# Performance work log

Hardware: AMD Instinct MI355X
Metric: run time of the kernel (lower is better)

The kernel has to match this reference:

```python
import jax, jax.numpy as jnp
import numpy as np

B, N, DIM = 4, 1024, 512
H, DH = 8, 64
INNER = H * DH
MLP = 2048
EPS = 1e-5


def layernorm(x, g, b):
    m = x.mean(-1, keepdims=True)
    v = ((x - m) ** 2).mean(-1, keepdims=True)
    return (x - m) / jnp.sqrt(v + EPS) * g + b


def setup_inputs() -> dict:
    key = jax.random.key(0)
    ks = jax.random.split(key, 12)
    s = 0.02
    return {
        "q": jax.random.normal(ks[0], (B, N, DIM), jnp.float32),
        "k": jax.random.normal(ks[1], (B, N, DIM), jnp.float32),
        "v": jax.random.normal(ks[2], (B, N, DIM), jnp.float32),
        "Win": jax.random.normal(ks[3], (INNER, DIM), jnp.float32) * s,
        "Wout": jax.random.normal(ks[4], (DIM, INNER), jnp.float32) * s,
        "bout": jnp.zeros((DIM,), jnp.float32),
        "g1": jnp.ones((DIM,), jnp.float32),
        "b1n": jnp.zeros((DIM,), jnp.float32),
        "g2": jnp.ones((DIM,), jnp.float32),
        "b2n": jnp.zeros((DIM,), jnp.float32),
        "Wup": jax.random.normal(ks[5], (MLP, DIM), jnp.float32) * s,
        "bup": jnp.zeros((MLP,), jnp.float32),
        "Wdn": jax.random.normal(ks[6], (DIM, MLP), jnp.float32) * s,
        "bdn": jnp.zeros((DIM,), jnp.float32),
        "wp_W1": jax.random.normal(ks[7], (DH, 2 * DH), jnp.float32) * s,
        "wp_b1": jnp.zeros((DH,), jnp.float32),
        "wp_g": jnp.ones((DH,), jnp.float32),
        "wp_b": jnp.zeros((DH,), jnp.float32),
        "wp_W2": jax.random.normal(ks[8], (3, DH), jnp.float32) * s,
        "wp_b2": jnp.zeros((3,), jnp.float32),
        "num_heads": H,
        "dim_head": DH,
        "mlp_dim": MLP,
    }


def reference(q, k, v, Win, Wout, bout, g1, b1n, g2, b2n, Wup, bup, Wdn, bdn,
              wp_W1, wp_b1, wp_g, wp_b, wp_W2, wp_b2, num_heads, dim_head, mlp_dim):
    b, n, _ = q.shape

    def split_heads(x):  # [b,n,dim] -> [h,b,n,d]
        f = x @ Win.T
        return f.reshape(b, n, num_heads, dim_head).transpose(2, 0, 1, 3)

    fq = split_heads(layernorm(q, g1, b1n))
    fk = split_heads(layernorm(k, g1, b1n))
    fv = split_heads(layernorm(v, g1, b1n))

    # cosine similarity component
    dots = jnp.einsum('hbnd,hbmd->hbnm', fq, fk)
    nq = jnp.linalg.norm(fq, axis=-1)  # [h,b,n]
    nk = jnp.linalg.norm(fk, axis=-1)  # [h,b,m]
    cosine_sim = dots / (nq[..., :, None] * nk[..., None, :])

    # mean-centered covariance component
    qc = fq - fq.mean(-1, keepdims=True)
    kc = fk - fk.mean(-1, keepdims=True)
    cov_component = jnp.einsum('hbnd,hbmd->hbnm', qc, kc) / dim_head

    # variance outer-product component (torch.var -> unbiased, ddof=1)
    qv = jnp.var(fq, axis=-1, ddof=1)  # [h,b,n]
    kv = jnp.var(fk, axis=-1, ddof=1)  # [h,b,m]
    var_component = qv[..., :, None] * kv[..., None, :] / dim_head

    # dynamic per-head mixing weights
    qg = fq.mean(axis=(1, 2))  # [h,d]
    kg = fk.mean(axis=(1, 2))
    feats = jnp.concatenate([qg, kg], axis=-1)  # [h,2d]
    h1 = jax.nn.relu(layernorm(feats @ wp_W1.T + wp_b1, wp_g, wp_b))
    w = jax.nn.softmax(h1 @ wp_W2.T + wp_b2, axis=-1)  # [h,3]
    cw = w[:, 0][:, None, None, None]
    covw = w[:, 1][:, None, None, None]
    vw = w[:, 2][:, None, None, None]

    scores = cw * cosine_sim + covw * cov_component + vw * var_component
    out = jnp.einsum('hbnm,hbmd->hbnd', scores, fv)
    out = out.transpose(1, 2, 0, 3).reshape(b, n, num_heads * dim_head)
    attn = out @ Wout.T + bout

    q2 = q + attn
    x = layernorm(q2, g2, b2n)
    y = jax.nn.gelu(x @ Wup.T + bup, approximate=False) @ Wdn.T + bdn
    return q2 + y
```

## Files before the change

kernel.cpp:

```cpp
#include <hip/hip_runtime.h>
#include <math.h>

#define EPS 1e-5f
#define ROWS 4096

typedef __attribute__((ext_vector_type(8))) short short8;
typedef __attribute__((ext_vector_type(4))) float floatx4;

__device__ inline short f2bf(float f) {
    unsigned u = __builtin_bit_cast(unsigned, f);
    unsigned r = (u + 0x7fffu + ((u >> 16) & 1u)) >> 16;
    return (short)r;
}

__global__ __launch_bounds__(256) void lnconv(
    const float* __restrict__ x0, const float* __restrict__ x1,
    const float* __restrict__ x2, const float* __restrict__ g,
    const float* __restrict__ bb, short* __restrict__ out) {
    int tensor = blockIdx.y;
    const float* x = tensor == 0 ? x0 : (tensor == 1 ? x1 : x2);
    int t = threadIdx.x;
    int row = blockIdx.x * 4 + (t >> 6);
    int col = (t & 63) * 8;
    const float* xr = x + (size_t)row * 512 + col;
    float4 v0 = *(const float4*)xr;
    float4 v1 = *(const float4*)(xr + 4);
    float s = v0.x + v0.y + v0.z + v0.w + v1.x + v1.y + v1.z + v1.w;
    float sq = v0.x * v0.x + v0.y * v0.y + v0.z * v0.z + v0.w * v0.w +
               v1.x * v1.x + v1.y * v1.y + v1.z * v1.z + v1.w * v1.w;
#pragma unroll
    for (int off = 32; off; off >>= 1) {
        s += __shfl_xor(s, off);
        sq += __shfl_xor(sq, off);
    }
    float m = s * (1.f / 512.f);
    float rstd = rsqrtf(sq * (1.f / 512.f) - m * m + EPS);
    float4 g0 = *(const float4*)(g + col);
    float4 g1 = *(const float4*)(g + col + 4);
    float4 b0 = *(const float4*)(bb + col);
    float4 b1 = *(const float4*)(bb + col + 4);
    short8 o;
    o[0] = f2bf((v0.x - m) * rstd * g0.x + b0.x);
    o[1] = f2bf((v0.y - m) * rstd * g0.y + b0.y);
    o[2] = f2bf((v0.z - m) * rstd * g0.z + b0.z);
    o[3] = f2bf((v0.w - m) * rstd * g0.w + b0.w);
    o[4] = f2bf((v1.x - m) * rstd * g1.x + b1.x);
    o[5] = f2bf((v1.y - m) * rstd * g1.y + b1.y);
    o[6] = f2bf((v1.z - m) * rstd * g1.z + b1.z);
    o[7] = f2bf((v1.w - m) * rstd * g1.w + b1.w);
    *(short8*)(out + (size_t)(tensor * 4096 + row) * 512 + col) = o;
}

__global__ void wconv(const float* __restrict__ w0, const float* __restrict__ w1,
                      const float* __restrict__ w2, const float* __restrict__ w3,
                      short* __restrict__ o0, short* __restrict__ o1,
                      short* __restrict__ o2, short* __restrict__ o3) {
    int y = blockIdx.y;
    const float* src = y == 0 ? w0 : (y == 1 ? w1 : (y == 2 ? w2 : w3));
    short* dst = y == 0 ? o0 : (y == 1 ? o1 : (y == 2 ? o2 : o3));
    int n = (y < 2) ? 262144 : 1048576;
    int idx = (blockIdx.x * 256 + threadIdx.x) * 8;
    if (idx < n) {
        float4 v0 = *(const float4*)(src + idx);
        float4 v1 = *(const float4*)(src + idx + 4);
        short8 o;
        o[0] = f2bf(v0.x); o[1] = f2bf(v0.y); o[2] = f2bf(v0.z); o[3] = f2bf(v0.w);
        o[4] = f2bf(v1.x); o[5] = f2bf(v1.y); o[6] = f2bf(v1.z); o[7] = f2bf(v1.w);
        *(short8*)(dst + idx) = o;
    }
}

template <int TM, int TN, int EPI, bool OUT_BF16>
__global__ __launch_bounds__(256) void mfma_gemm_nt(
    const short* __restrict__ A, const short* __restrict__ B,
    void* __restrict__ C, int M, int N, int K,
    const float* __restrict__ bias, const float* __restrict__ resid) {
    constexpr int FI = TM / 32;
    constexpr int FJ = TN / 32;
    __shared__ short As[TM * 32];
    __shared__ short Bs[TN * 32];
    int t = threadIdx.x;
    int m0 = blockIdx.y * TM, n0 = blockIdx.x * TN;
    int w = t >> 6, lane = t & 63;
    int wm = (w & 1) * (TM / 2), wn = (w >> 1) * (TN / 2);
    floatx4 acc[FI][FJ];
#pragma unroll
    for (int i = 0; i < FI; ++i)
#pragma unroll
        for (int j = 0; j < FJ; ++j) acc[i][j] = (floatx4){0.f, 0.f, 0.f, 0.f};

    int arow = t >> 2, acol = (t & 3) * 8;
    const short* Ag = A + (size_t)(m0 + arow) * K + acol;
    const short* Bg = B + (size_t)(n0 + arow) * K + acol;
    int ldsbase = w * 1024;

    for (int k0 = 0; k0 < K; k0 += 32) {
        __syncthreads();
#pragma unroll
        for (int u = 0; u < TM / 64; ++u)
            __builtin_amdgcn_global_load_lds(
                (const __attribute__((address_space(1))) void*)(Ag + (size_t)u * 64 * K + k0),
                (__attribute__((address_space(3))) void*)((char*)As + u * 4096 + ldsbase),
                16, 0, 0);
#pragma unroll
        for (int u = 0; u < TN / 64; ++u)
            __builtin_amdgcn_global_load_lds(
                (const __attribute__((address_space(1))) void*)(Bg + (size_t)u * 64 * K + k0),
                (__attribute__((address_space(3))) void*)((char*)Bs + u * 4096 + ldsbase),
                16, 0, 0);
        __syncthreads();
        int krow = (lane >> 4) * 8;
        short8 af[FI], bf[FJ];
#pragma unroll
        for (int i = 0; i < FI; ++i)
            af[i] = *(const short8*)&As[(wm + i * 16 + (lane & 15)) * 32 + krow];
#pragma unroll
        for (int j = 0; j < FJ; ++j)
            bf[j] = *(const short8*)&Bs[(wn + j * 16 + (lane & 15)) * 32 + krow];
#pragma unroll
        for (int i = 0; i < FI; ++i)
#pragma unroll
            for (int j = 0; j < FJ; ++j)
                acc[i][j] = __builtin_amdgcn_mfma_f32_16x16x32_bf16(
                    af[i], bf[j], acc[i][j], 0, 0, 0);
    }

    int col = lane & 15, rbase = (lane >> 4) * 4;
#pragma unroll
    for (int i = 0; i < FI; ++i) {
#pragma unroll
        for (int j = 0; j < FJ; ++j) {
            int gcol = n0 + wn + j * 16 + col;
#pragma unroll
            for (int r = 0; r < 4; ++r) {
                int grow = m0 + wm + i * 16 + rbase + r;
                float v = acc[i][j][r];
                if (EPI == 2) v += bias[gcol] + resid[(size_t)grow * N + gcol];
                if (EPI == 3) {
                    v += bias[gcol];
                    v = 0.5f * v * (1.f + erff(v * 0.70710678118654752f));
                }
                if (OUT_BF16)
                    ((short*)C)[(size_t)grow * N + gcol] = f2bf(v);
                else
                    ((float*)C)[(size_t)grow * N + gcol] = v;
            }
        }
    }
}

__global__ void head_stats2(const float* __restrict__ fq, const float* __restrict__ fk,
                            float* __restrict__ S) {
    int row = blockIdx.x;
    int y = blockIdx.y;
    const float* f = y ? fk : fq;
    float* base = S + (size_t)y * 98304;
    int t = threadIdx.x;
    int h = t >> 6, lane = t & 63;
    float v = f[(size_t)row * 512 + t];
    float s = v, sq = v * v;
#pragma unroll
    for (int off = 32; off; off >>= 1) {
        s += __shfl_xor(s, off);
        sq += __shfl_xor(sq, off);
    }
    if (lane == 0) {
        float m = s * (1.f / 64.f);
        int idx = h * ROWS + row;
        base[idx] = m;
        base[32768 + idx] = rsqrtf(sq);
        base[65536 + idx] = (sq - 64.f * m * m) * (1.f / 63.f);
    }
}

__global__ void zero_k(float* __restrict__ p, int n) {
    int i = blockIdx.x * blockDim.x + threadIdx.x;
    if (i < n) p[i] = 0.f;
}

__global__ void colmean(const float* __restrict__ fq, const float* __restrict__ fk,
                        float* __restrict__ qg, float* __restrict__ kg) {
    int tensor = blockIdx.y;
    const float* f = tensor ? fk : fq;
    float* o = tensor ? kg : qg;
    int col = threadIdx.x;
    int r0 = blockIdx.x * 32;
    float s = 0.f;
    for (int r = 0; r < 32; ++r) s += f[(size_t)(r0 + r) * 512 + col];
    atomicAdd(&o[col], s * (1.f / 4096.f));
}

__global__ void policy_mlp(const float* __restrict__ qg, const float* __restrict__ kg,
                           const float* __restrict__ W1, const float* __restrict__ b1,
                           const float* __restrict__ g, const float* __restrict__ bb,
                           const float* __restrict__ W2, const float* __restrict__ b2,
                           float* __restrict__ wmix) {
    int h = blockIdx.x, j = threadIdx.x;
    float acc = 0.f;
    const float* w1r = W1 + j * 128;
    for (int i = 0; i < 64; ++i) acc += qg[h * 64 + i] * w1r[i];
    for (int i = 0; i < 64; ++i) acc += kg[h * 64 + i] * w1r[64 + i];
    acc += b1[j];
    float s = acc, sq = acc * acc;
#pragma unroll
    for (int off = 32; off; off >>= 1) {
        s += __shfl_xor(s, off);
        sq += __shfl_xor(sq, off);
    }
    float m = s * (1.f / 64.f);
    float var = sq * (1.f / 64.f) - m * m;
    float xh = (acc - m) * rsqrtf(var + EPS) * g[j] + bb[j];
    float r = fmaxf(xh, 0.f);
    float l[3];
#pragma unroll
    for (int c = 0; c < 3; ++c) {
        float p = r * W2[c * 64 + j];
#pragma unroll
        for (int off = 32; off; off >>= 1) p += __shfl_xor(p, off);
        l[c] = p + b2[c];
    }
    if (j == 0) {
        float mx = fmaxf(l[0], fmaxf(l[1], l[2]));
        float e0 = expf(l[0] - mx), e1 = expf(l[1] - mx), e2 = expf(l[2] - mx);
        float inv = 1.f / (e0 + e1 + e2);
        wmix[h * 3 + 0] = e0 * inv;
        wmix[h * 3 + 1] = e1 * inv;
        wmix[h * 3 + 2] = e2 * inv;
    }
}

__global__ __launch_bounds__(256) void ksideP(
    const float* __restrict__ fk, const float* __restrict__ fv,
    const float* __restrict__ rnk, const float* __restrict__ kvv,
    const float* __restrict__ mk, float* __restrict__ Mpart) {
    int hb = blockIdx.x;
    int chunk = blockIdx.y;
    int h = hb >> 2, b = hb & 3;
    __shared__ float fkt[2048], fvt[2048];
    __shared__ float rs[32], kvs[32], mks[32];
    int t = threadIdx.x;
    int td = t >> 4, te = t & 15;
    float m1[4][4] = {}, m2[4][4] = {};
    float skv = 0.f, smk = 0.f;
    int mstart = chunk * 128;
    for (int m0 = mstart; m0 < mstart + 128; m0 += 32) {
        __syncthreads();
#pragma unroll
        for (int u = 0; u < 2; ++u) {
            int idx = u * 1024 + t * 4;
            int mm = idx >> 6, d = idx & 63;
            size_t grow = (size_t)(b * 1024 + m0 + mm) * 512 + h * 64 + d;
            *(float4*)&fkt[idx] = *(const float4*)&fk[grow];
            *(float4*)&fvt[idx] = *(const float4*)&fv[grow];
        }
        if (t < 32) {
            int sidx = h * ROWS + b * 1024 + m0 + t;
            rs[t] = rnk[sidx];
            kvs[t] = kvv[sidx];
            mks[t] = mk[sidx];
        }
        __syncthreads();
        for (int mi = 0; mi < 32; ++mi) {
            float r = rs[mi];
            float4 kq = *(const float4*)&fkt[mi * 64 + td * 4];
            float4 vq = *(const float4*)&fvt[mi * 64 + te * 4];
            float kr[4] = {kq.x, kq.y, kq.z, kq.w};
            float vr[4] = {vq.x, vq.y, vq.z, vq.w};
#pragma unroll
            for (int i = 0; i < 4; ++i) {
                float kv_ = kr[i], krr = kv_ * r;
#pragma unroll
                for (int j = 0; j < 4; ++j) {
                    m2[i][j] += kv_ * vr[j];
                    m1[i][j] += krr * vr[j];
                }
            }
            if (t < 64) {
                skv += kvs[mi] * fvt[mi * 64 + t];
                smk += mks[mi] * fvt[mi * 64 + t];
            }
        }
    }
    float* base = Mpart + (size_t)(chunk * 32 + hb) * 8320;
#pragma unroll
    for (int i = 0; i < 4; ++i)
#pragma unroll
        for (int j = 0; j < 4; ++j) {
            base[(td * 4 + i) * 64 + te * 4 + j] = m1[i][j];
            base[4096 + (td * 4 + i) * 64 + te * 4 + j] = m2[i][j];
        }
    if (t < 64) {
        base[8192 + t] = skv;
        base[8256 + t] = smk;
    }
}

__global__ void reduceM(const float* __restrict__ Mpart, float* __restrict__ Mbuf) {
    int i = blockIdx.x * 256 + threadIdx.x;
    if (i < 32 * 8320) {
        float s = 0.f;
#pragma unroll
        for (int c = 0; c < 8; ++c) s += Mpart[(size_t)c * 266240 + i];
        Mbuf[i] = s;
    }
}

__global__ __launch_bounds__(256) void qside(
    const float* __restrict__ fq, const float* __restrict__ Mbuf,
    const float* __restrict__ rnq, const float* __restrict__ mq,
    const float* __restrict__ qv, const float* __restrict__ wmix,
    short* __restrict__ attn_out) {
    int ntile = blockIdx.x, hb = blockIdx.y;
    int h = hb >> 2, b = hb & 3;
    __shared__ float M1s[4096], M2s[4096], fqt[4096];
    __shared__ float Skvs[64], Smks[64], rnqs[64], mqs[64], qvs[64];
    int t = threadIdx.x;
    const float* base = Mbuf + (size_t)hb * 8320;
#pragma unroll
    for (int u = 0; u < 4; ++u) {
        int idx = t * 4 + u * 1024;
        *(float4*)&M1s[idx] = *(const float4*)&base[idx];
        *(float4*)&M2s[idx] = *(const float4*)&base[4096 + idx];
    }
    int n0 = ntile * 64;
#pragma unroll
    for (int u = 0; u < 4; ++u) {
        int idx = t * 4 + u * 1024;
        int r = idx >> 6, d = idx & 63;
        *(float4*)&fqt[idx] = *(const float4*)&fq[(size_t)(b * 1024 + n0 + r) * 512 + h * 64 + d];
    }
    if (t < 64) {
        Skvs[t] = base[8192 + t];
        Smks[t] = base[8256 + t];
        int sidx = h * ROWS + b * 1024 + n0 + t;
        rnqs[t] = rnq[sidx];
        mqs[t] = mq[sidx];
        qvs[t] = qv[sidx];
    }
    __syncthreads();
    float cw = wmix[h * 3 + 0], covw = wmix[h * 3 + 1], vw = wmix[h * 3 + 2];
    int e = t & 63, rq = t >> 6;
    float a1[16] = {}, a2[16] = {};
    for (int d4 = 0; d4 < 64; d4 += 4) {
        float md1[4], md2[4];
#pragma unroll
        for (int dd = 0; dd < 4; ++dd) {
            md1[dd] = M1s[(d4 + dd) * 64 + e];
            md2[dd] = M2s[(d4 + dd) * 64 + e];
        }
#pragma unroll
        for (int i = 0; i < 16; ++i) {
            float4 f = *(const float4*)&fqt[(rq * 16 + i) * 64 + d4];
            a1[i] += f.x * md1[0] + f.y * md1[1] + f.z * md1[2] + f.w * md1[3];
            a2[i] += f.x * md2[0] + f.y * md2[1] + f.z * md2[2] + f.w * md2[3];
        }
    }
    float c2 = covw * (1.f / 64.f), c3 = vw * (1.f / 64.f);
#pragma unroll
    for (int i = 0; i < 16; ++i) {
        int rr = rq * 16 + i;
        float v = cw * rnqs[rr] * a1[i] + c2 * a2[i] + c3 * qvs[rr] * Skvs[e] -
                  covw * mqs[rr] * Smks[e];
        attn_out[(size_t)(b * 1024 + n0 + rr) * 512 + h * 64 + e] = f2bf(v);
    }
}

extern "C" void kernel_launch(void* const* d_in, const int* in_sizes, int n_in,
                              void* d_out, int out_size, void* d_ws, size_t ws_size,
                              hipStream_t stream) {
    const float* q = (const float*)d_in[0];
    const float* k = (const float*)d_in[1];
    const float* v = (const float*)d_in[2];
    const float* Win = (const float*)d_in[3];
    const float* Wout = (const float*)d_in[4];
    const float* bout = (const float*)d_in[5];
    const float* g1 = (const float*)d_in[6];
    const float* b1n = (const float*)d_in[7];
    const float* g2 = (const float*)d_in[8];
    const float* b2n = (const float*)d_in[9];
    const float* Wup = (const float*)d_in[10];
    const float* bup = (const float*)d_in[11];
    const float* Wdn = (const float*)d_in[12];
    const float* bdn = (const float*)d_in[13];
    const float* wpW1 = (const float*)d_in[14];
    const float* wpb1 = (const float*)d_in[15];
    const float* wpg = (const float*)d_in[16];
    const float* wpb = (const float*)d_in[17];
    const float* wpW2 = (const float*)d_in[18];
    const float* wpb2 = (const float*)d_in[19];
    float* out = (float*)d_out;

    float* wsf = (float*)d_ws;
    float* fq = wsf;
    float* fk = wsf + 2097152;
    float* fv = wsf + 2 * 2097152;
    short* hmid = (short*)wsf;
    short* qkvln = (short*)(wsf + 6291456);
    float* Mpart = wsf + 6291456;
    short* attnbf = (short*)(wsf + 6291456);
    short* x2bf = (short*)(wsf + 6291456 + 1048576);
    short* Winbf = (short*)(wsf + 9437184);
    short* Woutbf = (short*)(wsf + 9437184 + 131072);
    short* Wupbf = (short*)(wsf + 9437184 + 262144);
    short* Wdnbf = (short*)(wsf + 9437184 + 262144 + 524288);
    float* S = wsf + 10747904;
    float* qg = S + 196608;
    float* kg = qg + 512;
    float* Mbuf = kg + 512;
    float* wmix = Mbuf + 266240;
    float* mqS = S, *rnqS = S + 32768, *qvS = S + 65536;
    float* mkS = S + 98304, *rnkS = S + 131072, *kvS = S + 163840;

    wconv<<<dim3(512, 4), 256, 0, stream>>>(Win, Wout, Wup, Wdn,
                                            Winbf, Woutbf, Wupbf, Wdnbf);
    lnconv<<<dim3(1024, 3), 256, 0, stream>>>(q, k, v, g1, b1n, qkvln);
    zero_k<<<4, 256, 0, stream>>>(qg, 1024);

    mfma_gemm_nt<64, 128, 0, false><<<dim3(4, 192), 256, 0, stream>>>(
        qkvln, Winbf, fq, 12288, 512, 512, nullptr, nullptr);

    head_stats2<<<dim3(4096, 2), 512, 0, stream>>>(fq, fk, S);
    colmean<<<dim3(128, 2), 512, 0, stream>>>(fq, fk, qg, kg);
    policy_mlp<<<8, 64, 0, stream>>>(qg, kg, wpW1, wpb1, wpg, wpb, wpW2, wpb2, wmix);

    ksideP<<<dim3(32, 8), 256, 0, stream>>>(fk, fv, rnkS, kvS, mkS, Mpart);
    reduceM<<<1040, 256, 0, stream>>>(Mpart, Mbuf);
    qside<<<dim3(16, 32), 256, 0, stream>>>(fq, Mbuf, rnqS, mqS, qvS, wmix, attnbf);

    mfma_gemm_nt<64, 64, 2, false><<<dim3(8, 64), 256, 0, stream>>>(
        attnbf, Woutbf, out, 4096, 512, 512, bout, q);

    lnconv<<<dim3(1024, 1), 256, 0, stream>>>(out, out, out, g2, b2n, x2bf);
    mfma_gemm_nt<64, 128, 3, true><<<dim3(16, 64), 256, 0, stream>>>(
        x2bf, Wupbf, hmid, 4096, 2048, 512, bup, nullptr);
    mfma_gemm_nt<64, 128, 2, false><<<dim3(4, 64), 256, 0, stream>>>(
        hmid, Wdnbf, out, 4096, 512, 2048, bdn, out);
}
```

Measured before the change: 273.2 us.

## Fuse head stats with column mean, fold zeroing into wconv, retune GEMM tiles

Merges the per-row head statistics kernel and the column-mean kernel into one pass over fq/fk, so each element is read once instead of twice. The zero-init of qg/kg moves into the weight conversion kernel, removing one launch. GEMM tile shapes change for the QKV, output-projection and MLP-up GEMMs, giving fewer, larger blocks. The fused stats kernel now launches only 256 blocks, each looping over 32 rows, which lowers its parallelism. Larger tiles may also reduce occupancy.

```diff
diff --git a/kernel.cpp b/kernel.cpp
--- a/kernel.cpp
+++ b/kernel.cpp
@@ -54,8 +54,13 @@
 __global__ void wconv(const float* __restrict__ w0, const float* __restrict__ w1,
                       const float* __restrict__ w2, const float* __restrict__ w3,
                       short* __restrict__ o0, short* __restrict__ o1,
-                      short* __restrict__ o2, short* __restrict__ o3) {
+                      short* __restrict__ o2, short* __restrict__ o3,
+                      float* __restrict__ qgz) {
     int y = blockIdx.y;
+    if (y == 0) {
+        int zi = blockIdx.x * 256 + threadIdx.x;
+        if (zi < 1024) qgz[zi] = 0.f;
+    }
     const float* src = y == 0 ? w0 : (y == 1 ? w1 : (y == 2 ? w2 : w3));
     short* dst = y == 0 ? o0 : (y == 1 ? o1 : (y == 2 ? o2 : o3));
     int n = (y < 2) ? 262144 : 1048576;
@@ -149,45 +154,35 @@
     }
 }
 
-__global__ void head_stats2(const float* __restrict__ fq, const float* __restrict__ fk,
-                            float* __restrict__ S) {
-    int row = blockIdx.x;
+__global__ __launch_bounds__(512) void stats_fused(
+    const float* __restrict__ fq, const float* __restrict__ fk,
+    float* __restrict__ S, float* __restrict__ qg, float* __restrict__ kg) {
     int y = blockIdx.y;
     const float* f = y ? fk : fq;
     float* base = S + (size_t)y * 98304;
+    float* o = y ? kg : qg;
     int t = threadIdx.x;
     int h = t >> 6, lane = t & 63;
-    float v = f[(size_t)row * 512 + t];
-    float s = v, sq = v * v;
-#pragma unroll
-    for (int off = 32; off; off >>= 1) {
-        s += __shfl_xor(s, off);
-        sq += __shfl_xor(sq, off);
-    }
-    if (lane == 0) {
-        float m = s * (1.f / 64.f);
-        int idx = h * ROWS + row;
-        base[idx] = m;
-        base[32768 + idx] = rsqrtf(sq);
-        base[65536 + idx] = (sq - 64.f * m * m) * (1.f / 63.f);
-    }
-}
-
-__global__ void zero_k(float* __restrict__ p, int n) {
-    int i = blockIdx.x * blockDim.x + threadIdx.x;
-    if (i < n) p[i] = 0.f;
-}
-
-__global__ void colmean(const float* __restrict__ fq, const float* __restrict__ fk,
-                        float* __restrict__ qg, float* __restrict__ kg) {
-    int tensor = blockIdx.y;
-    const float* f = tensor ? fk : fq;
-    float* o = tensor ? kg : qg;
-    int col = threadIdx.x;
     int r0 = blockIdx.x * 32;
-    float s = 0.f;
-    for (int r = 0; r < 32; ++r) s += f[(size_t)(r0 + r) * 512 + col];
-    atomicAdd(&o[col], s * (1.f / 4096.f));
+    float csum = 0.f;
+    for (int r = 0; r < 32; ++r) {
+        float v = f[(size_t)(r0 + r) * 512 + t];
+        csum += v;
+        float s = v, sq = v * v;
+#pragma unroll
+        for (int off = 32; off; off >>= 1) {
+            s += __shfl_xor(s, off);
+            sq += __shfl_xor(sq, off);
+        }
+        if (lane == 0) {
+            float m = s * (1.f / 64.f);
+            int idx = h * ROWS + r0 + r;
+            base[idx] = m;
+            base[32768 + idx] = rsqrtf(sq);
+            base[65536 + idx] = (sq - 64.f * m * m) * (1.f / 63.f);
+        }
+    }
+    atomicAdd(&o[t], csum * (1.f / 4096.f));
 }
 
 __global__ void policy_mlp(const float* __restrict__ qg, const float* __restrict__ kg,
@@ -412,26 +407,24 @@
     float* mkS = S + 98304, *rnkS = S + 131072, *kvS = S + 163840;
 
     wconv<<<dim3(512, 4), 256, 0, stream>>>(Win, Wout, Wup, Wdn,
-                                            Winbf, Woutbf, Wupbf, Wdnbf);
+                                            Winbf, Woutbf, Wupbf, Wdnbf, qg);
     lnconv<<<dim3(1024, 3), 256, 0, stream>>>(q, k, v, g1, b1n, qkvln);
-    zero_k<<<4, 256, 0, stream>>>(qg, 1024);
-
-    mfma_gemm_nt<64, 128, 0, false><<<dim3(4, 192), 256, 0, stream>>>(
+
+    mfma_gemm_nt<128, 128, 0, false><<<dim3(4, 96), 256, 0, stream>>>(
         qkvln, Winbf, fq, 12288, 512, 512, nullptr, nullptr);
 
-    head_stats2<<<dim3(4096, 2), 512, 0, stream>>>(fq, fk, S);
-    colmean<<<dim3(128, 2), 512, 0, stream>>>(fq, fk, qg, kg);
+    stats_fused<<<dim3(128, 2), 512, 0, stream>>>(fq, fk, S, qg, kg);
     policy_mlp<<<8, 64, 0, stream>>>(qg, kg, wpW1, wpb1, wpg, wpb, wpW2, wpb2, wmix);
 
     ksideP<<<dim3(32, 8), 256, 0, stream>>>(fk, fv, rnkS, kvS, mkS, Mpart);
     reduceM<<<1040, 256, 0, stream>>>(Mpart, Mbuf);
     qside<<<dim3(16, 32), 256, 0, stream>>>(fq, Mbuf, rnqS, mqS, qvS, wmix, attnbf);
 
-    mfma_gemm_nt<64, 64, 2, false><<<dim3(8, 64), 256, 0, stream>>>(
+    mfma_gemm_nt<64, 128, 2, false><<<dim3(4, 64), 256, 0, stream>>>(
         attnbf, Woutbf, out, 4096, 512, 512, bout, q);
 
     lnconv<<<dim3(1024, 1), 256, 0, stream>>>(out, out, out, g2, b2n, x2bf);
-    mfma_gemm_nt<64, 128, 3, true><<<dim3(16, 64), 256, 0, stream>>>(
+    mfma_gemm_nt<128, 128, 3, true><<<dim3(16, 32), 256, 0, stream>>>(
         x2bf, Wupbf, hmid, 4096, 2048, 512, bup, nullptr);
     mfma_gemm_nt<64, 128, 2, false><<<dim3(4, 64), 256, 0, stream>>>(
         hmid, Wdnbf, out, 4096, 512, 2048, bdn, out);
```

New measurement: 283.8 us. 1.04x slower.
